# Performance work log

Measured on AMD Instinct MI355X. Metric: run time of the kernel, lower is better.

## Reference

```python
import jax, jax.numpy as jnp
import numpy as np

BN_EPS = 1e-5

def setup_inputs() -> dict:
    key = jax.random.key(0)
    ks = jax.random.split(key, 12)
    B, N, C, D = 8, 2048, 768, 384  # batch, tokens, high_dim, low_dim//reduc_ratio
    s_in = 1.0 / np.sqrt(C)
    s_out = 1.0 / np.sqrt(D)
    return {
        "x_h": jax.random.normal(ks[0], (B, N, C), jnp.float32),
        "x_l": jax.random.normal(ks[1], (B, N, C), jnp.float32),
        "w_g": jax.random.normal(ks[2], (D, C), jnp.float32) * s_in,
        "b_g": jax.random.normal(ks[3], (D,), jnp.float32) * s_in,
        "w_theta": jax.random.normal(ks[4], (D, C), jnp.float32) * s_in,
        "b_theta": jax.random.normal(ks[5], (D,), jnp.float32) * s_in,
        "w_phi": jax.random.normal(ks[6], (D, C), jnp.float32) * s_in,
        "b_phi": jax.random.normal(ks[7], (D,), jnp.float32) * s_in,
        "w_out": jax.random.normal(ks[8], (C, D), jnp.float32) * s_out,
        "b_out": jax.random.normal(ks[9], (C,), jnp.float32) * s_out,
        "bn_gamma": jax.random.normal(ks[10], (C,), jnp.float32),
        "bn_beta": jax.random.normal(ks[11], (C,), jnp.float32),
    }

def reference(x_h, x_l, w_g, b_g, w_theta, b_theta, w_phi, b_phi, w_out, b_out, bn_gamma, bn_beta):
    # 1x1 conv1d over channels == per-token linear
    g_x = jnp.einsum('bnc,dc->bnd', x_l, w_g) + b_g          # [B, N_l, D]
    theta_x = jnp.einsum('bnc,dc->bnd', x_h, w_theta) + b_theta  # [B, N_h, D]
    phi_x = jnp.einsum('bnc,dc->bnd', x_l, w_phi) + b_phi    # [B, N_l, D]
    n_l = phi_x.shape[1]
    energy = jnp.einsum('bnd,bmd->bnm', theta_x, phi_x)      # [B, N_h, N_l]
    attention = energy / n_l                                  # scalar normalization
    y = jnp.einsum('bnm,bmd->bnd', attention, g_x)           # [B, N_h, D]
    y = jnp.einsum('bnd,cd->bnc', y, w_out) + b_out          # [B, N_h, C]
    # BatchNorm1d (training mode): per-channel stats over batch and length dims
    mean = jnp.mean(y, axis=(0, 1))
    var = jnp.var(y, axis=(0, 1))
    y = bn_gamma * (y - mean) * jax.lax.rsqrt(var + BN_EPS) + bn_beta
    return y + x_h                                            # [B, N_h, C]
```

## Files before the change

### kernel.cpp

```cpp
#include <hip/hip_runtime.h>
#include <hip/hip_bf16.h>

typedef short bf16x8 __attribute__((ext_vector_type(8)));
typedef float f32x4 __attribute__((ext_vector_type(4)));

constexpr int Bb = 8, Ntok = 2048, Cdim = 768, Ddim = 384, Mrows = 16384;

__device__ __forceinline__ void gload16(const void* g, void* l) {
    __builtin_amdgcn_global_load_lds(
        (const __attribute__((address_space(1))) unsigned int*)g,
        (__attribute__((address_space(3))) unsigned int*)l, 16, 0, 0);
}

__device__ __forceinline__ unsigned short f2bf(float x) {
    union { float f; unsigned u; } c; c.f = x;
    const unsigned r = c.u + 0x7fffu + ((c.u >> 16) & 1u);
    return (unsigned short)(r >> 16);
}
__device__ __forceinline__ float bf2f(unsigned short u) {
    union { unsigned u; float f; } c; c.u = (unsigned)u << 16;
    return c.f;
}

__global__ __launch_bounds__(256) void cast_x(const float* __restrict__ s,
                                              unsigned short* __restrict__ d, int n8) {
    const int i = blockIdx.x * 256 + threadIdx.x;
    if (i >= n8) return;
    const float4* s4 = (const float4*)s;
    const float4 a = s4[2 * i], b = s4[2 * i + 1];
    union { unsigned short u[8]; uint4 q; } r;
    r.u[0] = f2bf(a.x); r.u[1] = f2bf(a.y); r.u[2] = f2bf(a.z); r.u[3] = f2bf(a.w);
    r.u[4] = f2bf(b.x); r.u[5] = f2bf(b.y); r.u[6] = f2bf(b.z); r.u[7] = f2bf(b.w);
    ((uint4*)d)[i] = r.q;
}

__global__ __launch_bounds__(256) void cast_w(const float* __restrict__ s0, const float* __restrict__ s1,
                                              const float* __restrict__ s2, const float* __restrict__ s3,
                                              unsigned short* __restrict__ d0, unsigned short* __restrict__ d1,
                                              unsigned short* __restrict__ d2, unsigned short* __restrict__ d3) {
    constexpr int n8 = 294912 / 8;
    const int i = blockIdx.x * 256 + threadIdx.x;
    const int sel = i / n8, loc = i - sel * n8;
    const float* s = sel == 0 ? s0 : sel == 1 ? s1 : sel == 2 ? s2 : s3;
    unsigned short* d = sel == 0 ? d0 : sel == 1 ? d1 : sel == 2 ? d2 : d3;
    const float4* s4 = (const float4*)s;
    const float4 a = s4[2 * loc], b = s4[2 * loc + 1];
    union { unsigned short u[8]; uint4 q; } r;
    r.u[0] = f2bf(a.x); r.u[1] = f2bf(a.y); r.u[2] = f2bf(a.z); r.u[3] = f2bf(a.w);
    r.u[4] = f2bf(b.x); r.u[5] = f2bf(b.y); r.u[6] = f2bf(b.z); r.u[7] = f2bf(b.w);
    ((uint4*)d)[loc] = r.q;
}

template <int OMODE, bool SPLITK>
__global__ __launch_bounds__(256) void gemm_bf16(
        const unsigned short* __restrict__ Abase, long sA,
        const unsigned short* __restrict__ Bbase, long sB,
        const float* __restrict__ bias, const float* __restrict__ bias2, int Nsplit,
        void* __restrict__ Cbase, long sC,
        int M, int N, int K, float scale,
        float* __restrict__ psumG, float* __restrict__ psqG) {
    constexpr int SMEM_BYTES = (OMODE == 2) ? 34304 : 32768;
    __shared__ __align__(16) char smem[SMEM_BYTES];

    const int tid  = threadIdx.x;
    const int lane = tid & 63;
    const int w    = tid >> 6;
    const int wm   = w >> 1, wn = w & 1;
    const int bm = blockIdx.y * 128, bn = blockIdx.x * 128;
    const int zz = blockIdx.z;

    int zb, kStart, kEnd;
    if constexpr (SPLITK) {
        zb = zz >> 2;
        const int kl = K >> 2;
        kStart = (zz & 3) * kl;
        kEnd = kStart + kl;
    } else {
        zb = zz; kStart = 0; kEnd = K;
    }

    const unsigned short* A = Abase + (size_t)zb * sA;
    const unsigned short* B = Bbase + (size_t)zb * sB;

    const int ldRow = tid >> 2;
    const int ldK   = (tid & 3) * 8;
    const unsigned ldsOff = tid * 16;
    const size_t aOff0 = (size_t)(bm + ldRow) * K + ldK;
    const size_t aOff1 = (size_t)(bm + 64 + ldRow) * K + ldK;
    const size_t bOff0 = (size_t)(bn + ldRow) * K + ldK;
    const size_t bOff1 = (size_t)(bn + 64 + ldRow) * K + ldK;

    f32x4 acc[4][4] = {};

    const int fr = lane & 15;
    const int fh = (lane >> 4) * 16;

    auto STAGE = [&](int p, int k0) {
        char* s = smem + p * 16384;
        gload16(A + aOff0 + k0, s + ldsOff);
        gload16(A + aOff1 + k0, s + 4096 + ldsOff);
        gload16(B + bOff0 + k0, s + 8192 + ldsOff);
        gload16(B + bOff1 + k0, s + 12288 + ldsOff);
    };

    STAGE(0, kStart);
    int it = 0;
    for (int k0 = kStart; k0 < kEnd; k0 += 32, ++it) {
        const int p = it & 1;
        const bool more = (k0 + 32 < kEnd);
        if (more) {
            STAGE(p ^ 1, k0 + 32);
            asm volatile("s_waitcnt vmcnt(4)" ::: "memory");
        } else {
            asm volatile("s_waitcnt vmcnt(0)" ::: "memory");
        }
        __syncthreads();
        const char* smA = smem + p * 16384;
        const char* smB = smA + 8192;
        bf16x8 fa[4], fb[4];
#pragma unroll
        for (int m = 0; m < 4; ++m)
            fa[m] = *(const bf16x8*)(smA + (wm * 64 + m * 16 + fr) * 64 + fh);
#pragma unroll
        for (int n = 0; n < 4; ++n)
            fb[n] = *(const bf16x8*)(smB + (wn * 64 + n * 16 + fr) * 64 + fh);
#pragma unroll
        for (int m = 0; m < 4; ++m)
#pragma unroll
            for (int n = 0; n < 4; ++n)
                acc[m][n] = __builtin_amdgcn_mfma_f32_16x16x32_bf16(fa[m], fb[n], acc[m][n], 0, 0, 0);
        __syncthreads();
    }

    const int r0 = (lane >> 4) * 4;
    const int cc = lane & 15;
    auto getbias = [&](int gcol) -> float {
        if (!bias) return 0.0f;
        return gcol < Nsplit ? bias[gcol] : bias2[gcol - Nsplit];
    };

    if constexpr (OMODE == 0) {
        float* C = (float*)Cbase + (size_t)(SPLITK ? zz : zb) * sC;
#pragma unroll
        for (int n = 0; n < 4; ++n) {
            const int col = bn + wn * 64 + n * 16 + cc;
            const float bv = getbias(col);
#pragma unroll
            for (int m = 0; m < 4; ++m)
#pragma unroll
                for (int j = 0; j < 4; ++j)
                    C[(size_t)(bm + wm * 64 + m * 16 + r0 + j) * N + col] = acc[m][n][j] + bv;
        }
    } else if constexpr (OMODE == 1) {
        unsigned short* C = (unsigned short*)Cbase + (size_t)zb * sC;
#pragma unroll
        for (int n = 0; n < 4; ++n) {
            const int col = bn + wn * 64 + n * 16 + cc;
            const float bv = getbias(col);
#pragma unroll
            for (int m = 0; m < 4; ++m)
#pragma unroll
                for (int j = 0; j < 4; ++j)
                    C[(size_t)(bm + wm * 64 + m * 16 + r0 + j) * N + col] =
                        f2bf(acc[m][n][j] * scale + bv);
        }
    } else if constexpr (OMODE == 2) {
        unsigned short* T = (unsigned short*)smem;
#pragma unroll
        for (int n = 0; n < 4; ++n) {
            const int ccol = wn * 64 + n * 16 + cc;
            const float bv = getbias(bn + ccol);
#pragma unroll
            for (int m = 0; m < 4; ++m)
#pragma unroll
                for (int j = 0; j < 4; ++j)
                    T[ccol * 134 + (wm * 64 + m * 16 + r0 + j)] = f2bf(acc[m][n][j] + bv);
        }
        __syncthreads();
        const int b   = bm >> 11;
        const int bmb = bm & 2047;
        unsigned short* Co = (unsigned short*)Cbase + (size_t)b * N * Ntok;
#pragma unroll
        for (int i = 0; i < 32; ++i) {
            const int d = w * 32 + i;
            const unsigned v = *(const unsigned*)((const char*)smem + d * 268 + lane * 4);
            *(unsigned*)(Co + (size_t)(bn + d) * Ntok + bmb + lane * 2) = v;
        }
    } else {
        unsigned short* C = (unsigned short*)Cbase + (size_t)zb * sC;
        float colS[4], colQ[4];
#pragma unroll
        for (int n = 0; n < 4; ++n) {
            const int col = bn + wn * 64 + n * 16 + cc;
            const float bv = getbias(col);
            float s = 0.f, q = 0.f;
#pragma unroll
            for (int m = 0; m < 4; ++m)
#pragma unroll
                for (int j = 0; j < 4; ++j) {
                    const float v = acc[m][n][j] + bv;
                    C[(size_t)(bm + wm * 64 + m * 16 + r0 + j) * N + col] = f2bf(v);
                    s += v; q = fmaf(v, v, q);
                }
            s += __shfl_xor(s, 16); s += __shfl_xor(s, 32);
            q += __shfl_xor(q, 16); q += __shfl_xor(q, 32);
            colS[n] = s; colQ[n] = q;
        }
        float* sums = (float*)smem;
        float* sqs  = sums + 256;
        if (lane < 16) {
#pragma unroll
            for (int n = 0; n < 4; ++n) {
                sums[wm * 128 + wn * 64 + n * 16 + cc] = colS[n];
                sqs [wm * 128 + wn * 64 + n * 16 + cc] = colQ[n];
            }
        }
        __syncthreads();
        if (tid < 128) {
            const int slot = zb * gridDim.y + blockIdx.y;
            psumG[(size_t)slot * Cdim + bn + tid] = sums[tid] + sums[128 + tid];
            psqG [(size_t)slot * Cdim + bn + tid] = sqs[tid]  + sqs[128 + tid];
        }
    }
}

__global__ __launch_bounds__(256) void reduce_mt(const float* __restrict__ part,
                                                 unsigned short* __restrict__ Mo) {
    const int i = blockIdx.x * 256 + threadIdx.x;
    const int e = i * 4;
    const int b = e / (Ddim * Ddim);
    const int r = e - b * (Ddim * Ddim);
    const float* base = part + (size_t)b * 4 * (Ddim * Ddim) + r;
    float4 s = *(const float4*)(base);
    const float4 s1 = *(const float4*)(base + 1 * Ddim * Ddim);
    const float4 s2 = *(const float4*)(base + 2 * Ddim * Ddim);
    const float4 s3 = *(const float4*)(base + 3 * Ddim * Ddim);
    s.x += s1.x + s2.x + s3.x; s.y += s1.y + s2.y + s3.y;
    s.z += s1.z + s2.z + s3.z; s.w += s1.w + s2.w + s3.w;
    constexpr float sc = 1.0f / (float)Ntok;
    union { unsigned short u[4]; uint2 q; } o;
    o.u[0] = f2bf(s.x * sc); o.u[1] = f2bf(s.y * sc);
    o.u[2] = f2bf(s.z * sc); o.u[3] = f2bf(s.w * sc);
    *(uint2*)(Mo + e) = o.q;
}

__global__ __launch_bounds__(256) void bn_finalize(const float* __restrict__ psum,
                                                   const float* __restrict__ psq,
                                                   const float* __restrict__ gamma,
                                                   const float* __restrict__ beta,
                                                   float* __restrict__ a,
                                                   float* __restrict__ bb) {
    const int c = blockIdx.x * 256 + threadIdx.x;
    if (c >= Cdim) return;
    float s = 0.f, q = 0.f;
    for (int b = 0; b < 128; ++b) { s += psum[(size_t)b * Cdim + c]; q += psq[(size_t)b * Cdim + c]; }
    const float mean = s * (1.0f / (float)Mrows);
    const float var  = fmaf(-mean, mean, q * (1.0f / (float)Mrows));
    const float inv  = rsqrtf(var + 1e-5f);
    const float gsc  = gamma[c] * inv;
    a[c]  = gsc;
    bb[c] = fmaf(-mean, gsc, beta[c]);
}

__global__ __launch_bounds__(256) void bn_apply(const unsigned short* __restrict__ y,
                                                const float* __restrict__ xh,
                                                const float* __restrict__ a,
                                                const float* __restrict__ bb,
                                                float* __restrict__ outp) {
    const size_t i = (size_t)blockIdx.x * 256 + threadIdx.x;
    union { uint4 q; unsigned short u[8]; } v; v.q = ((const uint4*)y)[i];
    const int c8 = (int)(i % (Cdim / 8));
    const float4 A0 = ((const float4*)a)[c8 * 2],  A1 = ((const float4*)a)[c8 * 2 + 1];
    const float4 B0 = ((const float4*)bb)[c8 * 2], B1 = ((const float4*)bb)[c8 * 2 + 1];
    const float4 X0 = ((const float4*)xh)[i * 2],  X1 = ((const float4*)xh)[i * 2 + 1];
    float4 o0, o1;
    o0.x = fmaf(A0.x, bf2f(v.u[0]), B0.x) + X0.x;
    o0.y = fmaf(A0.y, bf2f(v.u[1]), B0.y) + X0.y;
    o0.z = fmaf(A0.z, bf2f(v.u[2]), B0.z) + X0.z;
    o0.w = fmaf(A0.w, bf2f(v.u[3]), B0.w) + X0.w;
    o1.x = fmaf(A1.x, bf2f(v.u[4]), B1.x) + X1.x;
    o1.y = fmaf(A1.y, bf2f(v.u[5]), B1.y) + X1.y;
    o1.z = fmaf(A1.z, bf2f(v.u[6]), B1.z) + X1.z;
    o1.w = fmaf(A1.w, bf2f(v.u[7]), B1.w) + X1.w;
    ((float4*)outp)[i * 2]     = o0;
    ((float4*)outp)[i * 2 + 1] = o1;
}

extern "C" void kernel_launch(void* const* d_in, const int* in_sizes, int n_in,
                              void* d_out, int out_size, void* d_ws, size_t ws_size,
                              hipStream_t stream) {
    const float* x_h   = (const float*)d_in[0];
    const float* x_l   = (const float*)d_in[1];
    const float* w_g   = (const float*)d_in[2];
    const float* b_g   = (const float*)d_in[3];
    const float* w_th  = (const float*)d_in[4];
    const float* b_th  = (const float*)d_in[5];
    const float* w_ph  = (const float*)d_in[6];
    const float* b_ph  = (const float*)d_in[7];
    const float* w_out = (const float*)d_in[8];
    const float* b_out = (const float*)d_in[9];
    const float* gamma = (const float*)d_in[10];
    const float* beta  = (const float*)d_in[11];
    float* out = (float*)d_out;

    char* p = (char*)d_ws;
    unsigned short* Xbuf  = (unsigned short*)p; p += (size_t)Mrows * Cdim * 2;
    unsigned short* Wth16 = (unsigned short*)p; p += 294912 * 2;
    unsigned short* Wpg16 = (unsigned short*)p; p += 2 * 294912 * 2;
    unsigned short* Wout16= (unsigned short*)p; p += 294912 * 2;
    unsigned short* Tbuf  = (unsigned short*)p; p += (size_t)Mrows * Ddim * 2;
    unsigned short* PGT   = (unsigned short*)p; p += (size_t)Mrows * Cdim * 2;
    unsigned short* Mbuf  = (unsigned short*)p; p += (size_t)Bb * Ddim * Ddim * 2;
    unsigned short* QTbuf = (unsigned short*)p; p += (size_t)Bb * Cdim * Ddim * 2;
    float* psum = (float*)p; p += (size_t)128 * Cdim * 4;
    float* psq  = (float*)p; p += (size_t)128 * Cdim * 4;
    float* avec = (float*)p; p += Cdim * 4;
    float* bvec = (float*)p; p += Cdim * 4;
    float* part = (float*)Xbuf;
    unsigned short* Ybuf = Xbuf;

    dim3 blk(256);
    const int BIG = 1 << 30;

    cast_x<<<6144, blk, 0, stream>>>(x_h, Xbuf, 1572864);
    cast_w<<<576, blk, 0, stream>>>(w_th, w_ph, w_g, w_out,
                                    Wth16, Wpg16, Wpg16 + 294912, Wout16);
    gemm_bf16<1, false><<<dim3(3, 128, 1), blk, 0, stream>>>(
        Xbuf, 0, Wth16, 0, b_th, nullptr, BIG, Tbuf, 0, Mrows, Ddim, Cdim, 1.0f,
        nullptr, nullptr);
    cast_x<<<6144, blk, 0, stream>>>(x_l, Xbuf, 1572864);
    gemm_bf16<2, false><<<dim3(6, 128, 1), blk, 0, stream>>>(
        Xbuf, 0, Wpg16, 0, b_ph, b_g, Ddim, PGT, 0, Mrows, 2 * Ddim, Cdim, 1.0f,
        nullptr, nullptr);
    gemm_bf16<0, true><<<dim3(3, 3, 32), blk, 0, stream>>>(
        PGT, (long)2 * Ddim * Ntok,
        PGT + (size_t)Ddim * Ntok, (long)2 * Ddim * Ntok, nullptr, nullptr, BIG,
        part, (long)Ddim * Ddim, Ddim, Ddim, Ntok, 1.0f, nullptr, nullptr);
    reduce_mt<<<1152, blk, 0, stream>>>(part, Mbuf);
    gemm_bf16<1, false><<<dim3(3, 6, 8), blk, 0, stream>>>(
        Wout16, 0, Mbuf, (long)Ddim * Ddim, nullptr, nullptr, BIG,
        QTbuf, (long)Cdim * Ddim, Cdim, Ddim, Ddim, 1.0f, nullptr, nullptr);
    gemm_bf16<3, false><<<dim3(6, 16, 8), blk, 0, stream>>>(
        Tbuf, (long)Ntok * Ddim, QTbuf, (long)Cdim * Ddim, b_out, nullptr, BIG,
        Ybuf, (long)Ntok * Cdim, Ntok, Cdim, Ddim, 1.0f, psum, psq);
    bn_finalize<<<dim3(3), blk, 0, stream>>>(psum, psq, gamma, beta, avec, bvec);
    bn_apply<<<dim3(6144), blk, 0, stream>>>(Ybuf, x_h, avec, bvec, out);
}
```

Before: 174.1 us.

## Fuse fp32-to-bf16 input cast into projection GEMM A-tile loading

```diff
diff --git a/kernel.cpp b/kernel.cpp
--- a/kernel.cpp
+++ b/kernel.cpp
@@ -1,5 +1,4 @@
 #include <hip/hip_runtime.h>
-#include <hip/hip_bf16.h>
 
 typedef short bf16x8 __attribute__((ext_vector_type(8)));
 typedef float f32x4 __attribute__((ext_vector_type(4)));
@@ -21,17 +20,22 @@
     union { unsigned u; float f; } c; c.u = (unsigned)u << 16;
     return c.f;
 }
-
-__global__ __launch_bounds__(256) void cast_x(const float* __restrict__ s,
-                                              unsigned short* __restrict__ d, int n8) {
-    const int i = blockIdx.x * 256 + threadIdx.x;
-    if (i >= n8) return;
-    const float4* s4 = (const float4*)s;
-    const float4 a = s4[2 * i], b = s4[2 * i + 1];
+__device__ __forceinline__ uint4 cvt8(const float4 a, const float4 b) {
     union { unsigned short u[8]; uint4 q; } r;
     r.u[0] = f2bf(a.x); r.u[1] = f2bf(a.y); r.u[2] = f2bf(a.z); r.u[3] = f2bf(a.w);
     r.u[4] = f2bf(b.x); r.u[5] = f2bf(b.y); r.u[6] = f2bf(b.z); r.u[7] = f2bf(b.w);
-    ((uint4*)d)[i] = r.q;
+    return r.q;
+}
+
+__device__ __forceinline__ void fence_acq() {
+    __builtin_amdgcn_s_barrier();
+    asm volatile("" ::: "memory");
+    __builtin_amdgcn_sched_barrier(0);
+}
+__device__ __forceinline__ void fence_rel() {
+    __builtin_amdgcn_sched_barrier(0);
+    asm volatile("s_waitcnt lgkmcnt(0)" ::: "memory");
+    __builtin_amdgcn_s_barrier();
 }
 
 __global__ __launch_bounds__(256) void cast_w(const float* __restrict__ s0, const float* __restrict__ s1,
@@ -44,16 +48,12 @@
     const float* s = sel == 0 ? s0 : sel == 1 ? s1 : sel == 2 ? s2 : s3;
     unsigned short* d = sel == 0 ? d0 : sel == 1 ? d1 : sel == 2 ? d2 : d3;
     const float4* s4 = (const float4*)s;
-    const float4 a = s4[2 * loc], b = s4[2 * loc + 1];
-    union { unsigned short u[8]; uint4 q; } r;
-    r.u[0] = f2bf(a.x); r.u[1] = f2bf(a.y); r.u[2] = f2bf(a.z); r.u[3] = f2bf(a.w);
-    r.u[4] = f2bf(b.x); r.u[5] = f2bf(b.y); r.u[6] = f2bf(b.z); r.u[7] = f2bf(b.w);
-    ((uint4*)d)[loc] = r.q;
-}
-
-template <int OMODE, bool SPLITK>
+    ((uint4*)d)[loc] = cvt8(s4[2 * loc], s4[2 * loc + 1]);
+}
+
+template <int OMODE, bool SPLITK, bool AFP32>
 __global__ __launch_bounds__(256) void gemm_bf16(
-        const unsigned short* __restrict__ Abase, long sA,
+        const void* __restrict__ Abase_, long sA,
         const unsigned short* __restrict__ Bbase, long sB,
         const float* __restrict__ bias, const float* __restrict__ bias2, int Nsplit,
         void* __restrict__ Cbase, long sC,
@@ -79,8 +79,9 @@
         zb = zz; kStart = 0; kEnd = K;
     }
 
-    const unsigned short* A = Abase + (size_t)zb * sA;
     const unsigned short* B = Bbase + (size_t)zb * sB;
+    const float* Af = (const float*)Abase_ + (AFP32 ? (size_t)zb * sA : 0);
+    const unsigned short* Ah = (const unsigned short*)Abase_ + (AFP32 ? 0 : (size_t)zb * sA);
 
     const int ldRow = tid >> 2;
     const int ldK   = (tid & 3) * 8;
@@ -91,32 +92,60 @@
     const size_t bOff1 = (size_t)(bn + 64 + ldRow) * K + ldK;
 
     f32x4 acc[4][4] = {};
-
     const int fr = lane & 15;
     const int fh = (lane >> 4) * 16;
 
-    auto STAGE = [&](int p, int k0) {
-        char* s = smem + p * 16384;
-        gload16(A + aOff0 + k0, s + ldsOff);
-        gload16(A + aOff1 + k0, s + 4096 + ldsOff);
-        gload16(B + bOff0 + k0, s + 8192 + ldsOff);
-        gload16(B + bOff1 + k0, s + 12288 + ldsOff);
-    };
-
-    STAGE(0, kStart);
+    float4 na0, na1, na2, na3;
+
+    auto stageB = [&](int p, int k0) {
+        char* s = smem + 16384 + p * 8192;
+        gload16(B + bOff0 + k0, s + ldsOff);
+        gload16(B + bOff1 + k0, s + 4096 + ldsOff);
+    };
+    auto stageA_g = [&](int p, int k0) {
+        char* s = smem + p * 8192;
+        gload16(Ah + aOff0 + k0, s + ldsOff);
+        gload16(Ah + aOff1 + k0, s + 4096 + ldsOff);
+    };
+    auto loadA_f = [&](int k0) {
+        na0 = *(const float4*)(Af + aOff0 + k0);
+        na1 = *(const float4*)(Af + aOff0 + k0 + 4);
+        na2 = *(const float4*)(Af + aOff1 + k0);
+        na3 = *(const float4*)(Af + aOff1 + k0 + 4);
+    };
+    auto writeA_f = [&](int p) {
+        char* s = smem + p * 8192;
+        *(uint4*)(s + ldsOff)        = cvt8(na0, na1);
+        *(uint4*)(s + 4096 + ldsOff) = cvt8(na2, na3);
+    };
+
+    if constexpr (AFP32) {
+        loadA_f(kStart);
+        stageB(0, kStart);
+        writeA_f(0);
+    } else {
+        stageA_g(0, kStart);
+        stageB(0, kStart);
+    }
+
     int it = 0;
     for (int k0 = kStart; k0 < kEnd; k0 += 32, ++it) {
         const int p = it & 1;
         const bool more = (k0 + 32 < kEnd);
         if (more) {
-            STAGE(p ^ 1, k0 + 32);
-            asm volatile("s_waitcnt vmcnt(4)" ::: "memory");
+            if constexpr (AFP32) { loadA_f(k0 + 32); stageB(p ^ 1, k0 + 32); }
+            else { stageA_g(p ^ 1, k0 + 32); stageB(p ^ 1, k0 + 32); }
+        }
+        if (more) {
+            if constexpr (AFP32) asm volatile("s_waitcnt vmcnt(6)" ::: "memory");
+            else                 asm volatile("s_waitcnt vmcnt(4)" ::: "memory");
         } else {
             asm volatile("s_waitcnt vmcnt(0)" ::: "memory");
         }
-        __syncthreads();
-        const char* smA = smem + p * 16384;
-        const char* smB = smA + 8192;
+        asm volatile("s_waitcnt lgkmcnt(0)" ::: "memory");
+        fence_acq();
+        const char* smA = smem + p * 8192;
+        const char* smB = smem + 16384 + p * 8192;
         bf16x8 fa[4], fb[4];
 #pragma unroll
         for (int m = 0; m < 4; ++m)
@@ -129,7 +158,10 @@
 #pragma unroll
             for (int n = 0; n < 4; ++n)
                 acc[m][n] = __builtin_amdgcn_mfma_f32_16x16x32_bf16(fa[m], fb[n], acc[m][n], 0, 0, 0);
-        __syncthreads();
+        if constexpr (AFP32) {
+            if (more) writeA_f(p ^ 1);
+        }
+        fence_rel();
     }
 
     const int r0 = (lane >> 4) * 4;
@@ -304,7 +336,7 @@
     float* out = (float*)d_out;
 
     char* p = (char*)d_ws;
-    unsigned short* Xbuf  = (unsigned short*)p; p += (size_t)Mrows * Cdim * 2;
+    unsigned short* Scr   = (unsigned short*)p; p += (size_t)Mrows * Cdim * 2;
     unsigned short* Wth16 = (unsigned short*)p; p += 294912 * 2;
     unsigned short* Wpg16 = (unsigned short*)p; p += 2 * 294912 * 2;
     unsigned short* Wout16= (unsigned short*)p; p += 294912 * 2;
@@ -316,31 +348,29 @@
     float* psq  = (float*)p; p += (size_t)128 * Cdim * 4;
     float* avec = (float*)p; p += Cdim * 4;
     float* bvec = (float*)p; p += Cdim * 4;
-    float* part = (float*)Xbuf;
-    unsigned short* Ybuf = Xbuf;
+    float* part = (float*)Scr;
+    unsigned short* Ybuf = Scr;
 
     dim3 blk(256);
     const int BIG = 1 << 30;
 
-    cast_x<<<6144, blk, 0, stream>>>(x_h, Xbuf, 1572864);
     cast_w<<<576, blk, 0, stream>>>(w_th, w_ph, w_g, w_out,
                                     Wth16, Wpg16, Wpg16 + 294912, Wout16);
-    gemm_bf16<1, false><<<dim3(3, 128, 1), blk, 0, stream>>>(
-        Xbuf, 0, Wth16, 0, b_th, nullptr, BIG, Tbuf, 0, Mrows, Ddim, Cdim, 1.0f,
+    gemm_bf16<1, false, true><<<dim3(3, 128, 1), blk, 0, stream>>>(
+        x_h, 0, Wth16, 0, b_th, nullptr, BIG, Tbuf, 0, Mrows, Ddim, Cdim, 1.0f,
         nullptr, nullptr);
-    cast_x<<<6144, blk, 0, stream>>>(x_l, Xbuf, 1572864);
-    gemm_bf16<2, false><<<dim3(6, 128, 1), blk, 0, stream>>>(
-        Xbuf, 0, Wpg16, 0, b_ph, b_g, Ddim, PGT, 0, Mrows, 2 * Ddim, Cdim, 1.0f,
+    gemm_bf16<2, false, true><<<dim3(6, 128, 1), blk, 0, stream>>>(
+        x_l, 0, Wpg16, 0, b_ph, b_g, Ddim, PGT, 0, Mrows, 2 * Ddim, Cdim, 1.0f,
         nullptr, nullptr);
-    gemm_bf16<0, true><<<dim3(3, 3, 32), blk, 0, stream>>>(
+    gemm_bf16<0, true, false><<<dim3(3, 3, 32), blk, 0, stream>>>(
         PGT, (long)2 * Ddim * Ntok,
         PGT + (size_t)Ddim * Ntok, (long)2 * Ddim * Ntok, nullptr, nullptr, BIG,
         part, (long)Ddim * Ddim, Ddim, Ddim, Ntok, 1.0f, nullptr, nullptr);
     reduce_mt<<<1152, blk, 0, stream>>>(part, Mbuf);
-    gemm_bf16<1, false><<<dim3(3, 6, 8), blk, 0, stream>>>(
+    gemm_bf16<1, false, false><<<dim3(3, 6, 8), blk, 0, stream>>>(
         Wout16, 0, Mbuf, (long)Ddim * Ddim, nullptr, nullptr, BIG,
         QTbuf, (long)Cdim * Ddim, Cdim, Ddim, Ddim, 1.0f, nullptr, nullptr);
-    gemm_bf16<3, false><<<dim3(6, 16, 8), blk, 0, stream>>>(
+    gemm_bf16<3, false, false><<<dim3(6, 16, 8), blk, 0, stream>>>(
         Tbuf, (long)Ntok * Ddim, QTbuf, (long)Cdim * Ddim, b_out, nullptr, BIG,
         Ybuf, (long)Ntok * Cdim, Ntok, Cdim, Ddim, 1.0f, psum, psq);
     bn_finalize<<<dim3(3), blk, 0, stream>>>(psum, psq, gamma, beta, avec, bvec);
```

New measurement: 175.6 us. About the same (+0.8%).
